# Kernel tuning notes

Measured on AMD Instinct MI355X. Metric: run time of the kernel, lower is better.

## Reference

```python
import jax, jax.numpy as jnp
import numpy as np

LORA_SCALING = 1.0 / 2.0  # lora_alpha / lora_r = 1/2


def _qlora_linear(x, wq, A, B):
    # wq: (out, in/4) fake-NF4 compressed weight, repeated x4 -> (out, in)
    w = jnp.tile(wq, (1, 4))
    base = x @ w.T                              # (..., out)
    lora = (x @ A.T) @ B.T                      # low-rank path, r=2
    return base + lora * LORA_SCALING


def setup_inputs() -> dict:
    key = jax.random.key(0)
    ks = jax.random.split(key, 10)
    d, h, r = 4096, 11008, 2
    return {
        "x":   jax.random.normal(ks[0], (16, 1, d), dtype=jnp.float32),
        "w1q": jax.random.normal(ks[1], (h, d // 4), dtype=jnp.float32) * 0.02,
        "a1":  jax.random.normal(ks[2], (r, d), dtype=jnp.float32) * 0.02,
        "b1":  jax.random.normal(ks[3], (h, r), dtype=jnp.float32) * 0.02,
        "w3q": jax.random.normal(ks[4], (h, d // 4), dtype=jnp.float32) * 0.02,
        "a3":  jax.random.normal(ks[5], (r, d), dtype=jnp.float32) * 0.02,
        "b3":  jax.random.normal(ks[6], (h, r), dtype=jnp.float32) * 0.02,
        "w2q": jax.random.normal(ks[7], (d, h // 4), dtype=jnp.float32) * 0.02,
        "a2":  jax.random.normal(ks[8], (r, h), dtype=jnp.float32) * 0.02,
        "b2":  jax.random.normal(ks[9], (d, r), dtype=jnp.float32) * 0.02,
    }


def reference(x, w1q, a1, b1, w3q, a3, b3, w2q, a2, b2):
    # SwiGLU MLP: w2( silu(w1(x)) * w3(x) ), each linear = repeat-dequant + LoRA
    gate = jax.nn.silu(_qlora_linear(x, w1q, a1, b1))  # (B, S, hidden)
    up = _qlora_linear(x, w3q, a3, b3)                 # (B, S, hidden)
    return _qlora_linear(gate * up, w2q, a2, b2)       # (B, S, d_model)
```

## Files before the change

kernel.cpp:

```cpp
#include <hip/hip_runtime.h>
#include <hip/hip_bf16.h>


#define NB     16
#define DMODEL 4096
#define HID    11008
#define DQ     1024
#define HQ     2752

#define XSB_OFF 0
#define T1_OFF  8192
#define T3_OFF  8224
#define HVT_OFF 8256
#define HSB_OFF 184384
#define T2_OFF  206400

typedef __attribute__((ext_vector_type(8))) short bf16x8;
typedef __attribute__((ext_vector_type(4))) float f32x4;

__device__ __forceinline__ unsigned short f2bfh(float f) {
  __hip_bfloat16 h = __float2bfloat16(f);
  return __builtin_bit_cast(unsigned short, h);
}
__device__ __forceinline__ unsigned pack2(float lo, float hi) {
  return (unsigned)f2bfh(lo) | ((unsigned)f2bfh(hi) << 16);
}
__device__ __forceinline__ bf16x8 cvt8(const float4 a, const float4 b) {
  uint4 u = make_uint4(pack2(a.x, a.y), pack2(a.z, a.w),
                       pack2(b.x, b.y), pack2(b.z, b.w));
  return __builtin_bit_cast(bf16x8, u);
}

__global__ __launch_bounds__(256) void k_prep1(const float* __restrict__ x,
                                               const float* __restrict__ a1,
                                               const float* __restrict__ a3,
                                               float* __restrict__ ws) {
  const int b = blockIdx.x, t = threadIdx.x;
  if (b == 0 && t < 32) ws[T2_OFF + t] = 0.f;

  const float4* x4  = (const float4*)(x) + b * (DMODEL / 4);
  const float4* a14 = (const float4*)a1;
  const float4* a34 = (const float4*)a3;
  float4 xs = make_float4(0.f, 0.f, 0.f, 0.f);
  float s10 = 0.f, s11 = 0.f, s30 = 0.f, s31 = 0.f;
#pragma unroll
  for (int k = 0; k < 4; ++k) {
    float4 xv  = x4[k * 256 + t];
    xs.x += xv.x; xs.y += xv.y; xs.z += xv.z; xs.w += xv.w;
    float4 a10 = a14[k * 256 + t];
    float4 a11 = a14[1024 + k * 256 + t];
    float4 a30 = a34[k * 256 + t];
    float4 a31 = a34[1024 + k * 256 + t];
    s10 += xv.x * a10.x + xv.y * a10.y + xv.z * a10.z + xv.w * a10.w;
    s11 += xv.x * a11.x + xv.y * a11.y + xv.z * a11.z + xv.w * a11.w;
    s30 += xv.x * a30.x + xv.y * a30.y + xv.z * a30.z + xv.w * a30.w;
    s31 += xv.x * a31.x + xv.y * a31.y + xv.z * a31.z + xv.w * a31.w;
  }
  ((uint2*)(ws + XSB_OFF))[b * 256 + t] =
      make_uint2(pack2(xs.x, xs.y), pack2(xs.z, xs.w));

  __shared__ float4 rb[256];
  rb[t] = make_float4(s10, s11, s30, s31);
  __syncthreads();
  for (int s = 128; s > 0; s >>= 1) {
    if (t < s) {
      rb[t].x += rb[t + s].x; rb[t].y += rb[t + s].y;
      rb[t].z += rb[t + s].z; rb[t].w += rb[t + s].w;
    }
    __syncthreads();
  }
  if (t == 0) {
    ws[T1_OFF + b * 2]     = rb[0].x;
    ws[T1_OFF + b * 2 + 1] = rb[0].y;
    ws[T3_OFF + b * 2]     = rb[0].z;
    ws[T3_OFF + b * 2 + 1] = rb[0].w;
  }
}

__global__ __launch_bounds__(512) void k_gateup(const float* __restrict__ w1q,
                                                const float* __restrict__ w3q,
                                                const float* __restrict__ b1,
                                                const float* __restrict__ b3,
                                                const float* __restrict__ ws,
                                                float* __restrict__ hvecT) {
  __shared__ float red[8][8][64];
  const int t = threadIdx.x, w = t >> 6, l = t & 63;
  const int tile = blockIdx.x;
  const int n  = l & 15;
  const int kb = (l >> 4) * 8;
  const int o  = tile * 16 + n;
  const unsigned short* xsb = (const unsigned short*)(ws + XSB_OFF);

  f32x4 acc1 = {0.f, 0.f, 0.f, 0.f}, acc3 = {0.f, 0.f, 0.f, 0.f};
  const int k0 = w * 128;
#pragma unroll
  for (int kk = 0; kk < 4; ++kk) {
    const int kabs = k0 + kk * 32 + kb;
    const float4* p1 = (const float4*)(w1q + (size_t)o * DQ + kabs);
    const float4* p3 = (const float4*)(w3q + (size_t)o * DQ + kabs);
    const bf16x8 bb = *(const bf16x8*)(xsb + n * DQ + kabs);
    const bf16x8 a1f = cvt8(p1[0], p1[1]);
    const bf16x8 a3f = cvt8(p3[0], p3[1]);
    acc1 = __builtin_amdgcn_mfma_f32_16x16x32_bf16(a1f, bb, acc1, 0, 0, 0);
    acc3 = __builtin_amdgcn_mfma_f32_16x16x32_bf16(a3f, bb, acc3, 0, 0, 0);
  }
#pragma unroll
  for (int r = 0; r < 4; ++r) {
    red[w][r][l]     = acc1[r];
    red[w][r + 4][l] = acc3[r];
  }
  __syncthreads();
  if (w == 0) {
    const float t10 = ws[T1_OFF + 2 * n], t11 = ws[T1_OFF + 2 * n + 1];
    const float t30 = ws[T3_OFF + 2 * n], t31 = ws[T3_OFF + 2 * n + 1];
    const int m4 = (l >> 4) * 4;
#pragma unroll
    for (int r = 0; r < 4; ++r) {
      float g0 = 0.f, u0 = 0.f;
#pragma unroll
      for (int ww = 0; ww < 8; ++ww) {
        g0 += red[ww][r][l];
        u0 += red[ww][r + 4][l];
      }
      const int oo = tile * 16 + m4 + r;
      const float g = g0 + 0.5f * (t10 * b1[2 * oo] + t11 * b1[2 * oo + 1]);
      const float u = u0 + 0.5f * (t30 * b3[2 * oo] + t31 * b3[2 * oo + 1]);
      hvecT[oo * 16 + n] = (g / (1.f + __expf(-g))) * u;
    }
  }
}

__global__ __launch_bounds__(256) void k_prep2(const float* __restrict__ hvecT,
                                               const float* __restrict__ a2,
                                               float* __restrict__ ws) {
  const int t = threadIdx.x;
  const int b = t >> 4, jl = t & 15;
  const int j = blockIdx.x * 16 + jl;
  unsigned short* hsb = (unsigned short*)(ws + HSB_OFF);

  const float v0 = hvecT[(size_t)j * 16 + b];
  const float v1 = hvecT[(size_t)(j + HQ) * 16 + b];
  const float v2 = hvecT[(size_t)(j + 2 * HQ) * 16 + b];
  const float v3 = hvecT[(size_t)(j + 3 * HQ) * 16 + b];
  hsb[b * HQ + j] = f2bfh(v0 + v1 + v2 + v3);

  float s0 = v0 * a2[j] + v1 * a2[j + HQ] +
             v2 * a2[j + 2 * HQ] + v3 * a2[j + 3 * HQ];
  float s1 = v0 * a2[HID + j] + v1 * a2[HID + j + HQ] +
             v2 * a2[HID + j + 2 * HQ] + v3 * a2[HID + j + 3 * HQ];
#pragma unroll
  for (int off = 1; off < 16; off <<= 1) {
    s0 += __shfl_xor(s0, off);
    s1 += __shfl_xor(s1, off);
  }
  if (jl == 0) {
    atomicAdd(&ws[T2_OFF + 2 * b], s0);
    atomicAdd(&ws[T2_OFF + 2 * b + 1], s1);
  }
}

__global__ __launch_bounds__(512) void k_down(const float* __restrict__ w2q,
                                              const float* __restrict__ b2,
                                              const float* __restrict__ ws,
                                              float* __restrict__ out) {
  __shared__ float red[8][4][64];
  const int t = threadIdx.x, w = t >> 6, l = t & 63;
  const int tile = blockIdx.x;
  const int n  = l & 15;
  const int kb = (l >> 4) * 8;
  const int o  = tile * 16 + n;
  const unsigned short* hsb = (const unsigned short*)(ws + HSB_OFF);

  f32x4 acc = {0.f, 0.f, 0.f, 0.f};
  const int kks  = (w < 6) ? w * 11 : 66 + (w - 6) * 10;
  const int klen = (w < 6) ? 11 : 10;
#pragma unroll
  for (int kk = 0; kk < 11; ++kk) {
    if (kk < klen) {
      const int kabs = (kks + kk) * 32 + kb;
      const float4* p2 = (const float4*)(w2q + (size_t)o * HQ + kabs);
      const bf16x8 bb = *(const bf16x8*)(hsb + n * HQ + kabs);
      const bf16x8 af = cvt8(p2[0], p2[1]);
      acc = __builtin_amdgcn_mfma_f32_16x16x32_bf16(af, bb, acc, 0, 0, 0);
    }
  }
#pragma unroll
  for (int r = 0; r < 4; ++r) red[w][r][l] = acc[r];
  __syncthreads();
  if (w == 0) {
    const float t20 = ws[T2_OFF + 2 * n], t21 = ws[T2_OFF + 2 * n + 1];
    const int m4 = (l >> 4) * 4;
#pragma unroll
    for (int r = 0; r < 4; ++r) {
      float v = 0.f;
#pragma unroll
      for (int ww = 0; ww < 8; ++ww) v += red[ww][r][l];
      const int oo = tile * 16 + m4 + r;
      out[n * DMODEL + oo] = v + 0.5f * (t20 * b2[2 * oo] + t21 * b2[2 * oo + 1]);
    }
  }
}

extern "C" void kernel_launch(void* const* d_in, const int* in_sizes, int n_in,
                              void* d_out, int out_size, void* d_ws, size_t ws_size,
                              hipStream_t stream) {
  const float* x   = (const float*)d_in[0];
  const float* w1q = (const float*)d_in[1];
  const float* a1  = (const float*)d_in[2];
  const float* b1  = (const float*)d_in[3];
  const float* w3q = (const float*)d_in[4];
  const float* a3  = (const float*)d_in[5];
  const float* b3  = (const float*)d_in[6];
  const float* w2q = (const float*)d_in[7];
  const float* a2  = (const float*)d_in[8];
  const float* b2  = (const float*)d_in[9];
  float* out = (float*)d_out;
  float* ws  = (float*)d_ws;
  float* hvecT = ws + HVT_OFF;

  k_prep1<<<16, 256, 0, stream>>>(x, a1, a3, ws);
  k_gateup<<<HID / 16, 512, 0, stream>>>(w1q, w3q, b1, b3, ws, hvecT);
  k_prep2<<<HQ / 16, 256, 0, stream>>>(hvecT, a2, ws);
  k_down<<<DMODEL / 16, 512, 0, stream>>>(w2q, b2, ws, out);
}
```

Before: 49.96 us.

## Fuse prep2 into gate/up epilogue via atomics and split down-proj across two blocks

Removes the k_prep2 launch. The gate/up epilogue now atomically accumulates the folded hidden vector (fp32) and the LoRA A2 projection partials directly. The gate/up kernel moves to 256-thread blocks with 8 K-steps per wave. The down projection splits its K range across two 256-thread blocks per tile and combines them with atomicAdd into a zeroed output, converting the fp32 hidden vector to bf16 on the fly. This saves one launch and an intermediate round trip, at the cost of many atomics and zeroing the output and workspace in prep1.

```diff
diff --git a/kernel.cpp b/kernel.cpp
--- a/kernel.cpp
+++ b/kernel.cpp
@@ -11,9 +11,8 @@
 #define XSB_OFF 0
 #define T1_OFF  8192
 #define T3_OFF  8224
-#define HVT_OFF 8256
-#define HSB_OFF 184384
-#define T2_OFF  206400
+#define HF_OFF  8256
+#define T2_OFF  52288
 
 typedef __attribute__((ext_vector_type(8))) short bf16x8;
 typedef __attribute__((ext_vector_type(4))) float f32x4;
@@ -34,14 +33,20 @@
 __global__ __launch_bounds__(256) void k_prep1(const float* __restrict__ x,
                                                const float* __restrict__ a1,
                                                const float* __restrict__ a3,
-                                               float* __restrict__ ws) {
+                                               float* __restrict__ ws,
+                                               float* __restrict__ out) {
   const int b = blockIdx.x, t = threadIdx.x;
-  if (b == 0 && t < 32) ws[T2_OFF + t] = 0.f;
+  const int gid = b * 256 + t;
+  const float4 z4 = make_float4(0.f, 0.f, 0.f, 0.f);
+  for (int i = gid; i < 11016; i += 4096)
+    ((float4*)(ws + HF_OFF))[i] = z4;
+  for (int i = gid; i < 16384; i += 4096)
+    ((float4*)out)[i] = z4;
 
   const float4* x4  = (const float4*)(x) + b * (DMODEL / 4);
   const float4* a14 = (const float4*)a1;
   const float4* a34 = (const float4*)a3;
-  float4 xs = make_float4(0.f, 0.f, 0.f, 0.f);
+  float4 xs = z4;
   float s10 = 0.f, s11 = 0.f, s30 = 0.f, s31 = 0.f;
 #pragma unroll
   for (int k = 0; k < 4; ++k) {
@@ -77,13 +82,13 @@
   }
 }
 
-__global__ __launch_bounds__(512) void k_gateup(const float* __restrict__ w1q,
+__global__ __launch_bounds__(256) void k_gateup(const float* __restrict__ w1q,
                                                 const float* __restrict__ w3q,
                                                 const float* __restrict__ b1,
                                                 const float* __restrict__ b3,
-                                                const float* __restrict__ ws,
-                                                float* __restrict__ hvecT) {
-  __shared__ float red[8][8][64];
+                                                const float* __restrict__ a2,
+                                                float* __restrict__ ws) {
+  __shared__ float red[4][8][64];
   const int t = threadIdx.x, w = t >> 6, l = t & 63;
   const int tile = blockIdx.x;
   const int n  = l & 15;
@@ -92,9 +97,9 @@
   const unsigned short* xsb = (const unsigned short*)(ws + XSB_OFF);
 
   f32x4 acc1 = {0.f, 0.f, 0.f, 0.f}, acc3 = {0.f, 0.f, 0.f, 0.f};
-  const int k0 = w * 128;
-#pragma unroll
-  for (int kk = 0; kk < 4; ++kk) {
+  const int k0 = w * 256;
+#pragma unroll
+  for (int kk = 0; kk < 8; ++kk) {
     const int kabs = k0 + kk * 32 + kb;
     const float4* p1 = (const float4*)(w1q + (size_t)o * DQ + kabs);
     const float4* p3 = (const float4*)(w3q + (size_t)o * DQ + kabs);
@@ -114,73 +119,57 @@
     const float t10 = ws[T1_OFF + 2 * n], t11 = ws[T1_OFF + 2 * n + 1];
     const float t30 = ws[T3_OFF + 2 * n], t31 = ws[T3_OFF + 2 * n + 1];
     const int m4 = (l >> 4) * 4;
+    float p0 = 0.f, p1p = 0.f;
 #pragma unroll
     for (int r = 0; r < 4; ++r) {
       float g0 = 0.f, u0 = 0.f;
 #pragma unroll
-      for (int ww = 0; ww < 8; ++ww) {
+      for (int ww = 0; ww < 4; ++ww) {
         g0 += red[ww][r][l];
         u0 += red[ww][r + 4][l];
       }
       const int oo = tile * 16 + m4 + r;
       const float g = g0 + 0.5f * (t10 * b1[2 * oo] + t11 * b1[2 * oo + 1]);
       const float u = u0 + 0.5f * (t30 * b3[2 * oo] + t31 * b3[2 * oo + 1]);
-      hvecT[oo * 16 + n] = (g / (1.f + __expf(-g))) * u;
-    }
-  }
-}
-
-__global__ __launch_bounds__(256) void k_prep2(const float* __restrict__ hvecT,
-                                               const float* __restrict__ a2,
-                                               float* __restrict__ ws) {
-  const int t = threadIdx.x;
-  const int b = t >> 4, jl = t & 15;
-  const int j = blockIdx.x * 16 + jl;
-  unsigned short* hsb = (unsigned short*)(ws + HSB_OFF);
-
-  const float v0 = hvecT[(size_t)j * 16 + b];
-  const float v1 = hvecT[(size_t)(j + HQ) * 16 + b];
-  const float v2 = hvecT[(size_t)(j + 2 * HQ) * 16 + b];
-  const float v3 = hvecT[(size_t)(j + 3 * HQ) * 16 + b];
-  hsb[b * HQ + j] = f2bfh(v0 + v1 + v2 + v3);
-
-  float s0 = v0 * a2[j] + v1 * a2[j + HQ] +
-             v2 * a2[j + 2 * HQ] + v3 * a2[j + 3 * HQ];
-  float s1 = v0 * a2[HID + j] + v1 * a2[HID + j + HQ] +
-             v2 * a2[HID + j + 2 * HQ] + v3 * a2[HID + j + 3 * HQ];
-#pragma unroll
-  for (int off = 1; off < 16; off <<= 1) {
-    s0 += __shfl_xor(s0, off);
-    s1 += __shfl_xor(s1, off);
-  }
-  if (jl == 0) {
-    atomicAdd(&ws[T2_OFF + 2 * b], s0);
-    atomicAdd(&ws[T2_OFF + 2 * b + 1], s1);
-  }
-}
-
-__global__ __launch_bounds__(512) void k_down(const float* __restrict__ w2q,
+      const float v = (g / (1.f + __expf(-g))) * u;
+      const int jj = oo % HQ;
+      atomicAdd(&ws[HF_OFF + n * HQ + jj], v);
+      p0  += v * a2[oo];
+      p1p += v * a2[HID + oo];
+    }
+    p0  += __shfl_xor(p0, 16);  p0  += __shfl_xor(p0, 32);
+    p1p += __shfl_xor(p1p, 16); p1p += __shfl_xor(p1p, 32);
+    if (l < 16) {
+      atomicAdd(&ws[T2_OFF + 2 * n], p0);
+      atomicAdd(&ws[T2_OFF + 2 * n + 1], p1p);
+    }
+  }
+}
+
+__global__ __launch_bounds__(256) void k_down(const float* __restrict__ w2q,
                                               const float* __restrict__ b2,
                                               const float* __restrict__ ws,
                                               float* __restrict__ out) {
-  __shared__ float red[8][4][64];
+  __shared__ float red[4][4][64];
   const int t = threadIdx.x, w = t >> 6, l = t & 63;
-  const int tile = blockIdx.x;
+  const int tile = blockIdx.x >> 1, half = blockIdx.x & 1;
+  const int g = half * 4 + w;
   const int n  = l & 15;
   const int kb = (l >> 4) * 8;
   const int o  = tile * 16 + n;
-  const unsigned short* hsb = (const unsigned short*)(ws + HSB_OFF);
+  const float* hf = ws + HF_OFF;
 
   f32x4 acc = {0.f, 0.f, 0.f, 0.f};
-  const int kks  = (w < 6) ? w * 11 : 66 + (w - 6) * 10;
-  const int klen = (w < 6) ? 11 : 10;
+  const int kks  = (g < 6) ? g * 11 : 66 + (g - 6) * 10;
+  const int klen = (g < 6) ? 11 : 10;
 #pragma unroll
   for (int kk = 0; kk < 11; ++kk) {
     if (kk < klen) {
       const int kabs = (kks + kk) * 32 + kb;
       const float4* p2 = (const float4*)(w2q + (size_t)o * HQ + kabs);
-      const bf16x8 bb = *(const bf16x8*)(hsb + n * HQ + kabs);
+      const float4* pb = (const float4*)(hf + (size_t)n * HQ + kabs);
       const bf16x8 af = cvt8(p2[0], p2[1]);
+      const bf16x8 bb = cvt8(pb[0], pb[1]);
       acc = __builtin_amdgcn_mfma_f32_16x16x32_bf16(af, bb, acc, 0, 0, 0);
     }
   }
@@ -192,11 +181,11 @@
     const int m4 = (l >> 4) * 4;
 #pragma unroll
     for (int r = 0; r < 4; ++r) {
-      float v = 0.f;
-#pragma unroll
-      for (int ww = 0; ww < 8; ++ww) v += red[ww][r][l];
+      float v = red[0][r][l] + red[1][r][l] + red[2][r][l] + red[3][r][l];
       const int oo = tile * 16 + m4 + r;
-      out[n * DMODEL + oo] = v + 0.5f * (t20 * b2[2 * oo] + t21 * b2[2 * oo + 1]);
+      if (half == 0)
+        v += 0.5f * (t20 * b2[2 * oo] + t21 * b2[2 * oo + 1]);
+      atomicAdd(&out[n * DMODEL + oo], v);
     }
   }
 }
@@ -216,10 +205,8 @@
   const float* b2  = (const float*)d_in[9];
   float* out = (float*)d_out;
   float* ws  = (float*)d_ws;
-  float* hvecT = ws + HVT_OFF;
-
-  k_prep1<<<16, 256, 0, stream>>>(x, a1, a3, ws);
-  k_gateup<<<HID / 16, 512, 0, stream>>>(w1q, w3q, b1, b3, ws, hvecT);
-  k_prep2<<<HQ / 16, 256, 0, stream>>>(hvecT, a2, ws);
-  k_down<<<DMODEL / 16, 512, 0, stream>>>(w2q, b2, ws, out);
-}
+
+  k_prep1<<<16, 256, 0, stream>>>(x, a1, a3, ws, out);
+  k_gateup<<<HID / 16, 256, 0, stream>>>(w1q, w3q, b1, b3, a2, ws);
+  k_down<<<2 * (DMODEL / 16), 256, 0, stream>>>(w2q, b2, ws, out);
+}
```

After: 53.81 us. 1.08x slower.
